# Kernel optimization log

Hardware: AMD Instinct MI355X
Metric: run time of the kernel (lower is better)

Reference implementation:

```python
import jax, jax.numpy as jnp
import numpy as np

E, V, F, D = 500000, 50000, 100000, 128

def setup_inputs() -> dict:
    key = jax.random.key(0)
    ks = jax.random.split(key, 8)
    return {
        "prev_m_f_to_v": jax.random.normal(ks[0], (E, D), jnp.float32),
        "variable": jax.random.normal(ks[1], (V, D), jnp.float32),
        "factor": jax.random.normal(ks[2], (F, D), jnp.float32),
        "edge_attr": jax.random.normal(ks[3], (E, D), jnp.float32),
        "v_to_f": jax.random.randint(ks[4], (E,), 0, V, jnp.int32),
        "f_to_v": jax.random.randint(ks[5], (E,), 0, F, jnp.int32),
        "Wv": jax.random.normal(ks[6], (3 * D, D), jnp.float32) * (1.0 / np.sqrt(3 * D)),
        "bv": jnp.zeros((D,), jnp.float32),
        "Wf": jax.random.normal(ks[7], (3 * D, D), jnp.float32) * (1.0 / np.sqrt(3 * D)),
        "bf": jnp.zeros((D,), jnp.float32),
    }

def _mlp(x, y, edge_attr, W, b):
    # update(): concat along features then Linear(3d->d) + relu
    h = jnp.concatenate((x, y, edge_attr), axis=-1)  # [E, 3D]
    return jax.nn.relu(h @ W + b)                    # [E, D]

def reference(prev_m_f_to_v, variable, factor, edge_attr, v_to_f, f_to_v, Wv, bv, Wf, bf):
    nV = variable.shape[0]
    nF = factor.shape[0]
    # scatter-sum of factor->variable messages onto variables
    sum_f_to_v = jax.ops.segment_sum(prev_m_f_to_v, v_to_f, num_segments=nV)  # [V, D]
    # BP exclusion: gather back and subtract own message
    m_v_to_f = sum_f_to_v[v_to_f] - prev_m_f_to_v                             # [E, D]
    m_v_to_f = _mlp(variable[v_to_f], m_v_to_f, edge_attr, Wv, bv)            # [E, D]
    # scatter-sum of variable->factor messages onto factors
    sum_v_to_f = jax.ops.segment_sum(m_v_to_f, f_to_v, num_segments=nF)       # [F, D]
    m_f_to_v = sum_v_to_f[f_to_v] - m_v_to_f                                  # [E, D]
    m_f_to_v = _mlp(factor[f_to_v], m_f_to_v, edge_attr, Wf, bf)              # [E, D]
    new_factor = sum_v_to_f + factor
    new_variable = sum_f_to_v + variable
    return (m_f_to_v, new_factor, new_variable)
```

## Files before the change

kernel.cpp:

```cpp
#include <hip/hip_runtime.h>

typedef __attribute__((ext_vector_type(8))) __bf16 bf16x8;
typedef __attribute__((ext_vector_type(2))) __bf16 bf16x2;
typedef __attribute__((ext_vector_type(4))) float f32x4;

__device__ __forceinline__ void gload_lds16(const void* g, void* l) {
    __builtin_amdgcn_global_load_lds(
        (const __attribute__((address_space(1))) void*)g,
        (__attribute__((address_space(3))) void*)l, 16, 0, 0);
}

__device__ inline bf16x8 pack8(f32x4 u0, f32x4 u1) {
    bf16x8 r;
    r[0] = (__bf16)u0[0]; r[1] = (__bf16)u0[1]; r[2] = (__bf16)u0[2]; r[3] = (__bf16)u0[3];
    r[4] = (__bf16)u1[0]; r[5] = (__bf16)u1[1]; r[6] = (__bf16)u1[2]; r[7] = (__bf16)u1[3];
    return r;
}

__global__ void pack_w(const float* __restrict__ W, __bf16* __restrict__ out,
                       int baseA, float sA, int baseB, float sB) {
    int i = blockIdx.x * blockDim.x + threadIdx.x;
    if (i >= 256 * 128) return;
    int k = i >> 7, d = i & 127;
    float v = (k < 128) ? sA * W[(long)(baseA + k) * 128 + d]
                        : sB * W[(long)(baseB + (k - 128)) * 128 + d];
    int t = k >> 5, n = d >> 4;
    int lane = (d & 15) | (((k >> 3) & 3) << 4);
    int j = k & 7;
    out[((long)(t * 8 + n) * 64 + lane) * 8 + j] = (__bf16)v;
}


__global__ void hist_kernel(const int* __restrict__ v_to_f, const int* __restrict__ f_to_v,
                            int* __restrict__ counts, int V, int E) {
    int stride = gridDim.x * blockDim.x;
    for (int e = blockIdx.x * blockDim.x + threadIdx.x; e < E; e += stride) {
        atomicAdd(&counts[v_to_f[e]], 1);
        atomicAdd(&counts[V + f_to_v[e]], 1);
    }
}

#define SCAN_BLOCK 256
#define SCAN_ELEMS 4

__global__ void scan_pass1(const int* __restrict__ counts, int* __restrict__ partials, int N) {
    int t = threadIdx.x;
    int base = blockIdx.x * (SCAN_BLOCK * SCAN_ELEMS) + t * SCAN_ELEMS;
    int s = 0;
#pragma unroll
    for (int j = 0; j < SCAN_ELEMS; ++j) {
        int i = base + j;
        if (i < N) s += counts[i];
    }
#pragma unroll
    for (int off = 1; off < 64; off <<= 1) s += __shfl_xor(s, off);
    __shared__ int lds[4];
    if ((t & 63) == 0) lds[t >> 6] = s;
    __syncthreads();
    if (t == 0) partials[blockIdx.x] = lds[0] + lds[1] + lds[2] + lds[3];
}

__global__ void scan_pass2(int* __restrict__ partials, int nb, int* __restrict__ offsets,
                           int N, int total) {
    int t = threadIdx.x;
    int v = (t < nb) ? partials[t] : 0;
    int lane = t & 63, w = t >> 6;
    int x = v;
#pragma unroll
    for (int off = 1; off < 64; off <<= 1) { int y = __shfl_up(x, off); if (lane >= off) x += y; }
    __shared__ int lds[4];
    if (lane == 63) lds[w] = x;
    __syncthreads();
    int add = 0;
    for (int i = 0; i < w; ++i) add += lds[i];
    if (t < nb) partials[t] = x + add - v;
    if (t == 0) offsets[N] = total;
}

__global__ void scan_pass3(const int* __restrict__ counts, const int* __restrict__ partials,
                           int* __restrict__ offsets, int* __restrict__ cursors, int N) {
    int t = threadIdx.x;
    int base = blockIdx.x * (SCAN_BLOCK * SCAN_ELEMS) + t * SCAN_ELEMS;
    int c[SCAN_ELEMS];
    int s = 0;
#pragma unroll
    for (int j = 0; j < SCAN_ELEMS; ++j) {
        int i = base + j;
        c[j] = (i < N) ? counts[i] : 0;
        s += c[j];
    }
    int lane = t & 63, w = t >> 6;
    int x = s;
#pragma unroll
    for (int off = 1; off < 64; off <<= 1) { int y = __shfl_up(x, off); if (lane >= off) x += y; }
    __shared__ int lds[4];
    if (lane == 63) lds[w] = x;
    __syncthreads();
    int add = 0;
    for (int i = 0; i < w; ++i) add += lds[i];
    int run = x + add - s + partials[blockIdx.x];
#pragma unroll
    for (int j = 0; j < SCAN_ELEMS; ++j) {
        int i = base + j;
        if (i < N) { offsets[i] = run; cursors[i] = run; }
        run += c[j];
    }
}

__global__ void fill_kernel(const int* __restrict__ v_to_f, const int* __restrict__ f_to_v,
                            int* __restrict__ cursors, int* __restrict__ bucket, int V, int E) {
    int stride = gridDim.x * blockDim.x;
    for (int e = blockIdx.x * blockDim.x + threadIdx.x; e < E; e += stride) {
        int p = atomicAdd(&cursors[v_to_f[e]], 1);
        bucket[p] = e;
        int q = atomicAdd(&cursors[V + f_to_v[e]], 1);
        bucket[q] = e;
    }
}


__global__ __launch_bounds__(256) void gsum_f32(
    const float* __restrict__ src, const int* __restrict__ bucket,
    const int* __restrict__ offsets, int toff,
    const float* __restrict__ addtab, float* __restrict__ sumout,
    float* __restrict__ addout, int T) {
    int gw = (int)((blockIdx.x * (long)blockDim.x + threadIdx.x) >> 6);
    if (gw >= T) return;
    int lane = threadIdx.x & 63;
    int start = offsets[toff + gw], end = offsets[toff + gw + 1];
    float ax = 0.f, ay = 0.f, bx = 0.f, by = 0.f;
    int i = start;
    for (; i + 1 < end; i += 2) {
        int e0 = bucket[i], e1 = bucket[i + 1];
        float2 v0 = *(const float2*)(src + (long)e0 * 128 + lane * 2);
        float2 v1 = *(const float2*)(src + (long)e1 * 128 + lane * 2);
        ax += v0.x; ay += v0.y; bx += v1.x; by += v1.y;
    }
    if (i < end) {
        int e0 = bucket[i];
        float2 v0 = *(const float2*)(src + (long)e0 * 128 + lane * 2);
        ax += v0.x; ay += v0.y;
    }
    ax += bx; ay += by;
    long o = (long)gw * 128 + lane * 2;
    *(float2*)(sumout + o) = make_float2(ax, ay);
    float2 a = *(const float2*)(addtab + o);
    *(float2*)(addout + o) = make_float2(ax + a.x, ay + a.y);
}

__global__ __launch_bounds__(256) void gsum_bf16(
    const __bf16* __restrict__ src, const int* __restrict__ bucket,
    const int* __restrict__ offsets, int toff,
    const float* __restrict__ addtab, float* __restrict__ sumout,
    float* __restrict__ addout, int T) {
    int gw = (int)((blockIdx.x * (long)blockDim.x + threadIdx.x) >> 6);
    if (gw >= T) return;
    int lane = threadIdx.x & 63;
    int start = offsets[toff + gw], end = offsets[toff + gw + 1];
    float ax = 0.f, ay = 0.f, bx = 0.f, by = 0.f;
    int i = start;
    for (; i + 1 < end; i += 2) {
        int e0 = bucket[i], e1 = bucket[i + 1];
        bf16x2 v0 = *(const bf16x2*)(src + (long)e0 * 128 + lane * 2);
        bf16x2 v1 = *(const bf16x2*)(src + (long)e1 * 128 + lane * 2);
        ax += (float)v0[0]; ay += (float)v0[1];
        bx += (float)v1[0]; by += (float)v1[1];
    }
    if (i < end) {
        int e0 = bucket[i];
        bf16x2 v0 = *(const bf16x2*)(src + (long)e0 * 128 + lane * 2);
        ax += (float)v0[0]; ay += (float)v0[1];
    }
    ax += bx; ay += by;
    long o = (long)gw * 128 + lane * 2;
    *(float2*)(sumout + o) = make_float2(ax, ay);
    float2 a = *(const float2*)(addtab + o);
    *(float2*)(addout + o) = make_float2(ax + a.x, ay + a.y);
}

__global__ __launch_bounds__(256, 4) void table_gemm(
    const float* __restrict__ src0, const float* __restrict__ src1,
    const __bf16* __restrict__ WT, const float* __restrict__ bias,
    __bf16* __restrict__ out, int T) {
    const int wave = threadIdx.x >> 6;
    const int lane = threadIdx.x & 63;
    const int row = lane & 15;
    const int kch = lane >> 4;
    const long wbase = ((long)blockIdx.x * 4 + wave) * 32;

    const float* p0[2]; const float* p1[2];
#pragma unroll
    for (int rb = 0; rb < 2; ++rb) {
        long r = wbase + rb * 16 + row;
        long rl = (r < T) ? r : (T - 1);
        p0[rb] = src0 + rl * 128 + kch * 8;
        p1[rb] = src1 + rl * 128 + kch * 8;
    }

    f32x4 acc[8][2];
#pragma unroll
    for (int n = 0; n < 8; ++n) {
        acc[n][0] = (f32x4){0.f, 0.f, 0.f, 0.f};
        acc[n][1] = (f32x4){0.f, 0.f, 0.f, 0.f};
    }

#pragma unroll
    for (int t = 0; t < 8; ++t) {
        bf16x8 a[2];
#pragma unroll
        for (int rb = 0; rb < 2; ++rb) {
            const float* p = (t < 4) ? (p0[rb] + t * 32) : (p1[rb] + (t - 4) * 32);
            f32x4 u0 = *(const f32x4*)p;
            f32x4 u1 = *(const f32x4*)(p + 4);
            a[rb] = pack8(u0, u1);
        }
        const __bf16* bbase = WT + (long)t * 8 * 512 + lane * 8;
#pragma unroll
        for (int n = 0; n < 8; ++n) {
            bf16x8 b = *(const bf16x8*)(bbase + n * 512);
            acc[n][0] = __builtin_amdgcn_mfma_f32_16x16x32_bf16(a[0], b, acc[n][0], 0, 0, 0);
            acc[n][1] = __builtin_amdgcn_mfma_f32_16x16x32_bf16(a[1], b, acc[n][1], 0, 0, 0);
        }
    }

    const int colbase = lane & 15;
    const int orow = (lane >> 4) * 4;
#pragma unroll
    for (int n = 0; n < 8; ++n) {
        int col = n * 16 + colbase;
        float bz = bias[col];
#pragma unroll
        for (int rb = 0; rb < 2; ++rb)
#pragma unroll
            for (int rr = 0; rr < 4; ++rr) {
                long r = wbase + rb * 16 + orow + rr;
                if (r < T) out[r * 128 + col] = (__bf16)(acc[n][rb][rr] + bz);
            }
    }
}

template <int PHASE>
__global__ __launch_bounds__(256, 3) void edge_gemm(
    const float* __restrict__ prevf, const __bf16* __restrict__ prevb,
    const float* __restrict__ eattr, const __bf16* __restrict__ WT,
    const __bf16* __restrict__ G, const int* __restrict__ idx,
    __bf16* __restrict__ outb, float* __restrict__ outf, int E) {
    __shared__ char lds[3][16384];
    const int wave = threadIdx.x >> 6;
    const int lane = threadIdx.x & 63;
    const int row16 = lane & 15;
    const int kch = lane >> 4;
    const long brow = (long)blockIdx.x * 128;

    auto stage = [&](int buf, int t) {
        char* dst = &lds[buf][0];
        if (PHASE == 2 && t < 4) {
#pragma unroll
            for (int q = 0; q < 2; ++q) {
                int s0 = q * 256 + wave * 64;
                int row = (s0 >> 2) + (lane >> 2);
                int c = lane & 3;
                int c2 = c ^ ((row >> 1) & 3);
                long rowg = brow + row; if (rowg >= E) rowg = E - 1;
                gload_lds16(prevb + rowg * 128 + t * 32 + c2 * 8, dst + s0 * 16);
            }
        } else {
            const float* srcb = (PHASE == 1 && t < 4) ? (prevf + t * 32)
                                                      : (eattr + (t - 4) * 32);
#pragma unroll
            for (int q = 0; q < 4; ++q) {
                int s0 = q * 256 + wave * 64;
                int row = (s0 >> 3) + (lane >> 3);
                int c = lane & 7;
                int c2 = c ^ (row & 7);
                long rowg = brow + row; if (rowg >= E) rowg = E - 1;
                gload_lds16(srcb + rowg * 128 + c2 * 4, dst + s0 * 16);
            }
        }
    };

    const int orow = kch * 4;
    int gidx[2][4];
#pragma unroll
    for (int rb = 0; rb < 2; ++rb)
#pragma unroll
        for (int rr = 0; rr < 4; ++rr) {
            long eo = brow + wave * 32 + rb * 16 + orow + rr;
            gidx[rb][rr] = idx[(eo < E) ? eo : (E - 1)];
        }

    f32x4 acc[8][2];
#pragma unroll
    for (int n = 0; n < 8; ++n) {
        acc[n][0] = (f32x4){0.f, 0.f, 0.f, 0.f};
        acc[n][1] = (f32x4){0.f, 0.f, 0.f, 0.f};
    }

    stage(0, 0);
#pragma unroll
    for (int t = 0; t < 8; ++t) {
        __syncthreads();
        if (t < 7) stage((t + 1) % 3, t + 1);
        const char* cur = &lds[t % 3][0];
        bf16x8 a[2];
#pragma unroll
        for (int rb = 0; rb < 2; ++rb) {
            int row = wave * 32 + rb * 16 + row16;
            if (PHASE == 2 && t < 4) {
                int off = row * 64 + ((kch ^ ((row >> 1) & 3)) * 16);
                a[rb] = *(const bf16x8*)(cur + off);
            } else {
                int base = row * 128;
                int s0 = (((kch * 2 + 0) ^ (row & 7)) * 16);
                int s1 = (((kch * 2 + 1) ^ (row & 7)) * 16);
                f32x4 u0 = *(const f32x4*)(cur + base + s0);
                f32x4 u1 = *(const f32x4*)(cur + base + s1);
                a[rb] = pack8(u0, u1);
            }
        }
        const __bf16* bbase = WT + (long)t * 8 * 512 + lane * 8;
#pragma unroll
        for (int n = 0; n < 8; ++n) {
            bf16x8 b = *(const bf16x8*)(bbase + n * 512);
            acc[n][0] = __builtin_amdgcn_mfma_f32_16x16x32_bf16(a[0], b, acc[n][0], 0, 0, 0);
            acc[n][1] = __builtin_amdgcn_mfma_f32_16x16x32_bf16(a[1], b, acc[n][1], 0, 0, 0);
        }
    }

    const int colbase = lane & 15;
#pragma unroll
    for (int n = 0; n < 8; ++n) {
        int col = n * 16 + colbase;
#pragma unroll
        for (int rb = 0; rb < 2; ++rb)
#pragma unroll
            for (int rr = 0; rr < 4; ++rr) {
                long eo = brow + wave * 32 + rb * 16 + orow + rr;
                if (eo < E) {
                    float v = acc[n][rb][rr] + (float)G[(long)gidx[rb][rr] * 128 + col];
                    v = v > 0.f ? v : 0.f;
                    if (PHASE == 1) outb[eo * 128 + col] = (__bf16)v;
                    else            outf[eo * 128 + col] = v;
                }
            }
    }
}

extern "C" void kernel_launch(void* const* d_in, const int* in_sizes, int n_in,
                              void* d_out, int out_size, void* d_ws, size_t ws_size,
                              hipStream_t stream) {
    const float* prev_m   = (const float*)d_in[0];
    const float* variable = (const float*)d_in[1];
    const float* factor   = (const float*)d_in[2];
    const float* eattr    = (const float*)d_in[3];
    const int*   v_to_f   = (const int*)d_in[4];
    const int*   f_to_v   = (const int*)d_in[5];
    const float* Wv       = (const float*)d_in[6];
    const float* bv       = (const float*)d_in[7];
    const float* Wf       = (const float*)d_in[8];
    const float* bf       = (const float*)d_in[9];

    const int E = in_sizes[0] / 128;
    const int V = in_sizes[1] / 128;
    const int F = in_sizes[2] / 128;
    const int NT = V + F;

    float* out_m        = (float*)d_out;
    float* out_factor   = out_m + (long)E * 128;
    float* out_variable = out_factor + (long)F * 128;

    char* ws = (char*)d_ws;
    float* sum_f_to_v = (float*)ws;  ws += (long)V * 128 * 4;
    float* sum_v_to_f = (float*)ws;  ws += (long)F * 128 * 4;
    __bf16* m1        = (__bf16*)ws; ws += (long)E * 128 * 2;
    __bf16* G1        = (__bf16*)ws; ws += (long)V * 128 * 2;
    __bf16* G2        = (__bf16*)ws; ws += (long)F * 128 * 2;
    __bf16* Wtab_v    = (__bf16*)ws; ws += 256 * 128 * 2;
    __bf16* Wedge_v   = (__bf16*)ws; ws += 256 * 128 * 2;
    __bf16* Wtab_f    = (__bf16*)ws; ws += 256 * 128 * 2;
    __bf16* Wedge_f   = (__bf16*)ws; ws += 256 * 128 * 2;
    int* counts       = (int*)ws;    ws += (long)NT * 4;
    int* offsets      = (int*)ws;    ws += (long)(NT + 1) * 4;
    int* cursors      = (int*)ws;    ws += (long)NT * 4;
    int* bucket       = (int*)ws;    ws += (long)2 * E * 4;
    int* partials     = (int*)ws;    ws += 256 * 4;

    hipMemsetAsync(counts, 0, (size_t)NT * 4, stream);

    pack_w<<<dim3(128), dim3(256), 0, stream>>>(Wv, Wtab_v,  0,   1.f, 128, 1.f);
    pack_w<<<dim3(128), dim3(256), 0, stream>>>(Wv, Wedge_v, 128, -1.f, 256, 1.f);
    pack_w<<<dim3(128), dim3(256), 0, stream>>>(Wf, Wtab_f,  0,   1.f, 128, 1.f);
    pack_w<<<dim3(128), dim3(256), 0, stream>>>(Wf, Wedge_f, 128, -1.f, 256, 1.f);

    hist_kernel<<<dim3(2048), dim3(256), 0, stream>>>(v_to_f, f_to_v, counts, V, E);
    int nb = (NT + SCAN_BLOCK * SCAN_ELEMS - 1) / (SCAN_BLOCK * SCAN_ELEMS);
    scan_pass1<<<dim3(nb), dim3(SCAN_BLOCK), 0, stream>>>(counts, partials, NT);
    scan_pass2<<<dim3(1), dim3(SCAN_BLOCK), 0, stream>>>(partials, nb, offsets, NT, 2 * E);
    scan_pass3<<<dim3(nb), dim3(SCAN_BLOCK), 0, stream>>>(counts, partials, offsets, cursors, NT);
    fill_kernel<<<dim3(2048), dim3(256), 0, stream>>>(v_to_f, f_to_v, cursors, bucket, V, E);

    gsum_f32<<<dim3((V + 3) / 4), dim3(256), 0, stream>>>(
        prev_m, bucket, offsets, 0, variable, sum_f_to_v, out_variable, V);

    table_gemm<<<dim3((V + 127) / 128), dim3(256), 0, stream>>>(
        variable, sum_f_to_v, Wtab_v, bv, G1, V);

    int eblocks = (E + 127) / 128;
    edge_gemm<1><<<dim3(eblocks), dim3(256), 0, stream>>>(
        prev_m, nullptr, eattr, Wedge_v, G1, v_to_f, m1, nullptr, E);

    gsum_bf16<<<dim3((F + 3) / 4), dim3(256), 0, stream>>>(
        m1, bucket, offsets, V, factor, sum_v_to_f, out_factor, F);

    table_gemm<<<dim3((F + 127) / 128), dim3(256), 0, stream>>>(
        factor, sum_v_to_f, Wtab_f, bf, G2, F);

    edge_gemm<2><<<dim3(eblocks), dim3(256), 0, stream>>>(
        nullptr, m1, eattr, Wedge_f, G2, f_to_v, nullptr, out_m, E);
}
```

Baseline: 861.0 us.

## Stage edge GEMM epilogue through LDS for vectorized gathers and stores

The epilogue now writes MFMA accumulators into a swizzled per-wave LDS tile, then reads them back row-major so each lane handles four contiguous columns. This turns scalar 2/4-byte gathers of G and scalar output stores into 8/16-byte vector accesses, and it loads the index per row on demand. The LDS pipeline also drops from triple to double buffering, and launch bounds rise to 4 blocks per CU to raise occupancy. The costs are an extra LDS round trip, an extra barrier, less prefetch depth in the K loop, and more register pressure under the tighter bound.

Result: faster. 718.0 us (-16.6%).

```diff
diff --git a/kernel.cpp b/kernel.cpp
--- a/kernel.cpp
+++ b/kernel.cpp
@@ -1,6 +1,7 @@
 #include <hip/hip_runtime.h>
 
 typedef __attribute__((ext_vector_type(8))) __bf16 bf16x8;
+typedef __attribute__((ext_vector_type(4))) __bf16 bf16x4;
 typedef __attribute__((ext_vector_type(2))) __bf16 bf16x2;
 typedef __attribute__((ext_vector_type(4))) float f32x4;
 
@@ -240,15 +241,15 @@
 }
 
 template <int PHASE>
-__global__ __launch_bounds__(256, 3) void edge_gemm(
+__global__ __launch_bounds__(256, 4) void edge_gemm(
     const float* __restrict__ prevf, const __bf16* __restrict__ prevb,
     const float* __restrict__ eattr, const __bf16* __restrict__ WT,
     const __bf16* __restrict__ G, const int* __restrict__ idx,
     __bf16* __restrict__ outb, float* __restrict__ outf, int E) {
-    __shared__ char lds[3][16384];
+    __shared__ char lds[2][16384];
     const int wave = threadIdx.x >> 6;
     const int lane = threadIdx.x & 63;
-    const int row16 = lane & 15;
+    const int l16 = lane & 15;
     const int kch = lane >> 4;
     const long brow = (long)blockIdx.x * 128;
 
@@ -279,16 +280,6 @@
         }
     };
 
-    const int orow = kch * 4;
-    int gidx[2][4];
-#pragma unroll
-    for (int rb = 0; rb < 2; ++rb)
-#pragma unroll
-        for (int rr = 0; rr < 4; ++rr) {
-            long eo = brow + wave * 32 + rb * 16 + orow + rr;
-            gidx[rb][rr] = idx[(eo < E) ? eo : (E - 1)];
-        }
-
     f32x4 acc[8][2];
 #pragma unroll
     for (int n = 0; n < 8; ++n) {
@@ -300,12 +291,12 @@
 #pragma unroll
     for (int t = 0; t < 8; ++t) {
         __syncthreads();
-        if (t < 7) stage((t + 1) % 3, t + 1);
-        const char* cur = &lds[t % 3][0];
+        if (t < 7) stage((t + 1) & 1, t + 1);
+        const char* cur = &lds[t & 1][0];
         bf16x8 a[2];
 #pragma unroll
         for (int rb = 0; rb < 2; ++rb) {
-            int row = wave * 32 + rb * 16 + row16;
+            int row = wave * 32 + rb * 16 + l16;
             if (PHASE == 2 && t < 4) {
                 int off = row * 64 + ((kch ^ ((row >> 1) & 3)) * 16);
                 a[rb] = *(const bf16x8*)(cur + off);
@@ -327,22 +318,45 @@
         }
     }
 
-    const int colbase = lane & 15;
-#pragma unroll
-    for (int n = 0; n < 8; ++n) {
-        int col = n * 16 + colbase;
-#pragma unroll
-        for (int rb = 0; rb < 2; ++rb)
+    __syncthreads();
+    float* lbuf = (float*)((char*)lds + wave * 8192);
+    const int slotcol = lane & 31;
+    const int rhalf = lane >> 5;
+#pragma unroll
+    for (int rb = 0; rb < 2; ++rb) {
+#pragma unroll
+        for (int n = 0; n < 8; ++n)
 #pragma unroll
             for (int rr = 0; rr < 4; ++rr) {
-                long eo = brow + wave * 32 + rb * 16 + orow + rr;
-                if (eo < E) {
-                    float v = acc[n][rb][rr] + (float)G[(long)gidx[rb][rr] * 128 + col];
-                    v = v > 0.f ? v : 0.f;
-                    if (PHASE == 1) outb[eo * 128 + col] = (__bf16)v;
-                    else            outf[eo * 128 + col] = v;
+                int row = kch * 4 + rr;
+                int col = n * 16 + l16;
+                int slot = col >> 2;
+                lbuf[row * 128 + (((slot ^ (row & 7)) << 2) | (col & 3))] = acc[n][rb][rr];
+            }
+#pragma unroll
+        for (int j = 0; j < 8; ++j) {
+            int row = 2 * j + rhalf;
+            long eo = brow + wave * 32 + rb * 16 + row;
+            f32x4 v = *(const f32x4*)&lbuf[row * 128 + ((slotcol ^ (row & 7)) << 2)];
+            if (eo < E) {
+                int g = idx[eo];
+                bf16x4 gb = *(const bf16x4*)(G + (long)g * 128 + slotcol * 4);
+                f32x4 o;
+#pragma unroll
+                for (int i = 0; i < 4; ++i) {
+                    float x = v[i] + (float)gb[i];
+                    o[i] = x > 0.f ? x : 0.f;
                 }
-            }
+                if (PHASE == 1) {
+                    bf16x4 ob;
+#pragma unroll
+                    for (int i = 0; i < 4; ++i) ob[i] = (__bf16)o[i];
+                    *(bf16x4*)(outb + eo * 128 + slotcol * 4) = ob;
+                } else {
+                    *(f32x4*)(outf + eo * 128 + slotcol * 4) = o;
+                }
+            }
+        }
     }
 }
 
```
